# Kernel optimization log

Measured on AMD Instinct MI355X. Metric: run time of the kernel, lower is better.

Reference implementation:

```python
import jax, jax.numpy as jnp
import numpy as np


def _sliding_window_attention(q, k, v, window_size, padding_mask):
    # q,k,v: [B,H,S,D]; faithful to the torch code incl. clamped scatter_add
    # duplicates at boundaries and the (score==0 -> -inf) quirk.
    B, H, S, D = q.shape
    hw = window_size // 2
    kp = jnp.pad(k, ((0, 0), (0, 0), (hw, hw), (0, 0)))  # zero-pad seq dim
    # window gather positions into padded keys: [S, W+1]
    pos = jnp.arange(S)[:, None] + jnp.arange(window_size + 1)[None, :]
    kw = kp[:, :, pos, :]  # [B,H,S,W+1,D]
    scores = jnp.einsum('bhsd,bhswd->bhsw', q, kw) / jnp.sqrt(jnp.asarray(D, q.dtype))
    # scatter-add into full [B,H,S,S] with clamped column indices (duplicates sum)
    idx = jnp.clip(jnp.arange(S)[:, None] + jnp.arange(-hw, hw + 1)[None, :], 0, S - 1)  # [S,W+1]
    rows = jnp.arange(S)[:, None]
    full = jnp.zeros((B, H, S, S), q.dtype).at[:, :, rows, idx].add(scores)
    neg_inf = jnp.asarray(-jnp.inf, full.dtype)
    full = jnp.where(full == 0.0, neg_inf, full)
    if padding_mask is not None:
        pm = padding_mask[:, None, None, :]  # [B,1,1,S]
        full = jnp.where(pm == 0, neg_inf, full)
        full = jnp.where(jnp.swapaxes(pm, -1, -2) == 0, neg_inf, full)
    att = jax.nn.softmax(full, axis=-1)
    att = jnp.where(jnp.isnan(att), jnp.asarray(0.0, att.dtype), att)
    values = jnp.einsum('bhst,bhtd->bhsd', att, v)
    return values, att


def setup_inputs() -> dict:
    key = jax.random.key(0)
    ks = jax.random.split(key, 5)
    B, S, IN_DIM, E = 2, 2048, 512, 512
    x = jax.random.normal(ks[0], (B, S, IN_DIM), dtype=jnp.float32)
    padding_mask = jnp.ones((B, S), dtype=jnp.int32)
    qkv_w = jax.random.normal(ks[1], (3 * E, IN_DIM), dtype=jnp.float32) * 0.02
    qkv_b = jnp.zeros((3 * E,), dtype=jnp.float32)
    o_w = jax.random.normal(ks[2], (E, E), dtype=jnp.float32) * 0.02
    o_b = jnp.zeros((E,), dtype=jnp.float32)
    return {'x': x, 'padding_mask': padding_mask, 'qkv_w': qkv_w, 'qkv_b': qkv_b,
            'o_w': o_w, 'o_b': o_b, 'window_size': 256, 'num_heads': 8}


def reference(x, padding_mask, qkv_w, qkv_b, o_w, o_b, window_size, num_heads):
    B, S, _ = x.shape
    E3 = qkv_w.shape[0]
    E = E3 // 3
    head_dim = E // num_heads
    qkv = x @ qkv_w.T + qkv_b                         # [B,S,3E]
    qkv = qkv.reshape(B, S, num_heads, 3 * head_dim)
    qkv = jnp.transpose(qkv, (0, 2, 1, 3))            # [B,H,S,3*hd]
    q, k, v = jnp.split(qkv, 3, axis=-1)
    values, _ = _sliding_window_attention(q, k, v, window_size, padding_mask)
    values = jnp.transpose(values, (0, 2, 1, 3)).reshape(B, S, E)
    o = values @ o_w.T + o_b
    return o
```

## Files before the change

### kernel.cpp

```cpp
#include <hip/hip_runtime.h>
#include <hip/hip_bf16.h>
#include <math.h>


typedef __bf16 bf16x8 __attribute__((ext_vector_type(8)));
typedef float f32x4 __attribute__((ext_vector_type(4)));

__device__ __forceinline__ unsigned short f2bf(float f) {
  unsigned u = __float_as_uint(f);
  unsigned r = u + 0x7FFFu + ((u >> 16) & 1u);
  return (unsigned short)(r >> 16);
}

__device__ __forceinline__ void ldsdma16(void* lds, const void* g) {
  __builtin_amdgcn_global_load_lds(
      (const __attribute__((address_space(1))) unsigned int*)g,
      (__attribute__((address_space(3))) unsigned int*)lds, 16, 0, 0);
}

__global__ __launch_bounds__(256) void cvt3_kernel(
    const float* __restrict__ s0, unsigned short* __restrict__ d0, int n0,
    const float* __restrict__ s1, unsigned short* __restrict__ d1, int n1,
    const float* __restrict__ s2, unsigned short* __restrict__ d2, int n2) {
  int i4 = blockIdx.x * 256 + threadIdx.x;
  const int c0 = n0 >> 2, c1 = (n0 + n1) >> 2, c2 = (n0 + n1 + n2) >> 2;
  const float* s; unsigned short* d; int base4;
  if (i4 < c0)      { s = s0; d = d0; base4 = i4; }
  else if (i4 < c1) { s = s1; d = d1; base4 = i4 - c0; }
  else if (i4 < c2) { s = s2; d = d2; base4 = i4 - c1; }
  else return;
  float4 v = ((const float4*)s)[base4];
  ushort4 o;
  o.x = f2bf(v.x); o.y = f2bf(v.y); o.z = f2bf(v.z); o.w = f2bf(v.w);
  ((ushort4*)d)[base4] = o;
}

__global__ __launch_bounds__(256) void gemm_qkv(
    const __hip_bfloat16* __restrict__ A, const __hip_bfloat16* __restrict__ Bw,
    const float* __restrict__ bias,
    __hip_bfloat16* __restrict__ qp, __hip_bfloat16* __restrict__ kpb,
    unsigned short* __restrict__ vtb) {
  __shared__ __hip_bfloat16 As[128 * 32];
  __shared__ __hip_bfloat16 Bs[128 * 32];

  const int tid = threadIdx.x, wave = tid >> 6, lane = tid & 63;
  const int m0 = blockIdx.x * 128, n0 = blockIdx.y * 128;
  const int wm = (wave >> 1) * 64, wn = (wave & 1) * 64;
  const int cl = lane & 15, ko = (lane >> 4) * 8;
  const int srow = wave * 16 + (lane >> 2);
  const int scol = (lane & 3) * 8;

  f32x4 acc[4][4] = {};

  for (int k0 = 0; k0 < 512; k0 += 32) {
    __syncthreads();
    ldsdma16(&As[wave * 512],        A  + (size_t)(m0 + srow) * 512 + k0 + scol);
    ldsdma16(&As[2048 + wave * 512], A  + (size_t)(m0 + 64 + srow) * 512 + k0 + scol);
    ldsdma16(&Bs[wave * 512],        Bw + (size_t)(n0 + srow) * 512 + k0 + scol);
    ldsdma16(&Bs[2048 + wave * 512], Bw + (size_t)(n0 + 64 + srow) * 512 + k0 + scol);
    __syncthreads();

    bf16x8 af[4], bf[4];
#pragma unroll
    for (int i = 0; i < 4; i++)
      af[i] = *(const bf16x8*)(&As[(wm + cl + i * 16) * 32 + ko]);
#pragma unroll
    for (int i = 0; i < 4; i++)
      bf[i] = *(const bf16x8*)(&Bs[(wn + cl + i * 16) * 32 + ko]);
#pragma unroll
    for (int mi = 0; mi < 4; mi++)
#pragma unroll
      for (int ni = 0; ni < 4; ni++)
        acc[mi][ni] = __builtin_amdgcn_mfma_f32_16x16x32_bf16(
            af[mi], bf[ni], acc[mi][ni], 0, 0, 0);
  }

  const int crow = (lane >> 4) * 4;
#pragma unroll
  for (int mi = 0; mi < 4; mi++) {
    const int mb = m0 + wm + mi * 16 + crow;
    const int bq = mb >> 11, sl = mb & 2047;
#pragma unroll
    for (int ni = 0; ni < 4; ni++) {
      const int n = n0 + wn + ni * 16 + cl;
      const int h = n / 192;
      const int rem = n - h * 192;
      const int cat = rem >> 6;
      const int d = rem & 63;
      const float bv = bias[n];
      const size_t bh = (size_t)bq * 8 + h;
      if (cat == 2) {
        ushort4 o;
        o.x = f2bf(acc[mi][ni][0] + bv);
        o.y = f2bf(acc[mi][ni][1] + bv);
        o.z = f2bf(acc[mi][ni][2] + bv);
        o.w = f2bf(acc[mi][ni][3] + bv);
        *(ushort4*)(vtb + bh * 131072 + (sl >> 3) * 512 + d * 8 + (sl & 7)) = o;
      } else {
        __hip_bfloat16* dst = (cat == 0) ? qp : kpb;
        const float sc = (cat == 0) ? 0.18033688011112042f : 1.0f;
#pragma unroll
        for (int r = 0; r < 4; r++)
          dst[(bh * 2048 + sl + r) * 64 + d] =
              __float2bfloat16((acc[mi][ni][r] + bv) * sc);
      }
    }
  }
}

__global__ __launch_bounds__(256) void attn_mfma(
    const __hip_bfloat16* __restrict__ qp, const __hip_bfloat16* __restrict__ kp,
    const __hip_bfloat16* __restrict__ vt, const int* __restrict__ pm,
    __hip_bfloat16* __restrict__ vals) {
  __shared__ __hip_bfloat16 sKP[320 * 72];
  __shared__ float sCM[320];

  const int tid = threadIdx.x, wave = tid >> 6, lane = tid & 63;
  const int bid = blockIdx.x;
  const int s0 = (bid & 31) * 64;
  const int bh = bid >> 5;
  const int b = bh >> 3, h = bh & 7;
  const int t0 = s0 - 128;
  const int cl = lane & 15;
  const int g4 = (lane >> 4) * 4;
  const int ko = (lane >> 4) * 8;

  {
    const int e = (tid & 7) * 8;
#pragma unroll
    for (int i = 0; i < 10; i++) {
      int row = (tid >> 3) + i * 32;
      int t = t0 + row; t = min(max(t, 0), 2047);
      *(uint4*)(&sKP[row * 72 + e]) =
          *(const uint4*)(kp + ((size_t)bh * 2048 + t) * 64 + e);
    }
  }
  for (int c = tid; c < 320; c += 256) {
    int t = t0 + c;
    bool ok = (t >= 0 && t < 2048) && (pm[b * 2048 + t] != 0);
    sCM[c] = ok ? 0.0f : -3.0e38f;
  }
  __syncthreads();

  const __hip_bfloat16* qrow =
      qp + ((size_t)bh * 2048 + s0 + wave * 16 + cl) * 64 + ko;
  bf16x8 aq0 = *(const bf16x8*)(qrow);
  bf16x8 aq1 = *(const bf16x8*)(qrow + 32);

  f32x4 acc[17];
#pragma unroll
  for (int i = 0; i < 17; i++) {
    const int krow = (wave + i) * 16 + cl;
    bf16x8 b0 = *(const bf16x8*)(&sKP[krow * 72 + ko]);
    bf16x8 b1 = *(const bf16x8*)(&sKP[krow * 72 + ko + 32]);
    f32x4 z = {};
    z = __builtin_amdgcn_mfma_f32_16x16x32_bf16(aq0, b0, z, 0, 0, 0);
    acc[i] = __builtin_amdgcn_mfma_f32_16x16x32_bf16(aq1, b1, z, 0, 0, 0);
  }

  float mrow[4] = {-3.0e38f, -3.0e38f, -3.0e38f, -3.0e38f};
#pragma unroll
  for (int i = 0; i < 17; i++) {
    const float ca = sCM[(wave + i) * 16 + cl];
#pragma unroll
    for (int r = 0; r < 4; r++) {
      float sv = acc[i][r] + ca;
      if (i == 0) {
        if (cl < g4 + r) sv = -3.0e38f;
      } else if (i == 16) {
        if (cl > g4 + r) sv = -3.0e38f;
      }
      acc[i][r] = sv;
      mrow[r] = fmaxf(mrow[r], sv);
    }
  }
#pragma unroll
  for (int r = 0; r < 4; r++)
#pragma unroll
    for (int off = 1; off < 16; off <<= 1)
      mrow[r] = fmaxf(mrow[r], __shfl_xor(mrow[r], off));

  float lsum[4] = {0.f, 0.f, 0.f, 0.f};
#pragma unroll
  for (int i = 0; i < 17; i++)
#pragma unroll
    for (int r = 0; r < 4; r++) {
      float p = exp2f(acc[i][r] - mrow[r]);
      acc[i][r] = p;
      lsum[r] += p;
    }
#pragma unroll
  for (int r = 0; r < 4; r++)
#pragma unroll
    for (int off = 1; off < 16; off <<= 1)
      lsum[r] += __shfl_xor(lsum[r], off);

  __syncthreads();

  __hip_bfloat16* sp = sKP + wave * 5248;
#pragma unroll
  for (int i = 0; i < 17; i++) {
    const int c = (wave + i) * 16 + cl;
#pragma unroll
    for (int r = 0; r < 4; r++)
      sp[(g4 + r) * 328 + c] = __float2bfloat16(acc[i][r]);
  }
  {
    const int zt = (wave & 1) ? (wave - 1) : (wave + 17);
    const int zc = zt * 16 + cl;
#pragma unroll
    for (int r = 0; r < 4; r++)
      sp[(g4 + r) * 328 + zc] = __float2bfloat16(0.f);
  }

  f32x4 oacc[4] = {};
  const int k0 = wave >> 1;
  const __hip_bfloat16* vbase = vt + (size_t)bh * 131072;
#pragma unroll
  for (int ks = 0; ks < 9; ks++) {
    const int kk = (k0 + ks) * 32 + ko;
    bf16x8 pa = *(const bf16x8*)(&sp[cl * 328 + kk]);
    int tv = t0 + kk; tv = min(max(tv, 0), 2040);
    const __hip_bfloat16* vrow = vbase + (tv >> 3) * 512;
#pragma unroll
    for (int ni = 0; ni < 4; ni++) {
      const int d = ni * 16 + cl;
      bf16x8 vb = *(const bf16x8*)(vrow + d * 8);
      oacc[ni] = __builtin_amdgcn_mfma_f32_16x16x32_bf16(pa, vb, oacc[ni], 0, 0, 0);
    }
  }

#pragma unroll
  for (int r = 0; r < 4; r++) {
    float linv = 1.0f / fmaxf(lsum[r], 1e-20f);
    const int qr = wave * 16 + g4 + r;
    if (sCM[qr + 128] != 0.0f) linv = 0.0f;
    const size_t obase = ((size_t)(b * 2048 + s0 + qr)) * 512 + h * 64 + cl;
#pragma unroll
    for (int ni = 0; ni < 4; ni++)
      vals[obase + ni * 16] = __float2bfloat16(oacc[ni][r] * linv);
  }
}

__global__ __launch_bounds__(256) void gemm_out(
    const __hip_bfloat16* __restrict__ A, const __hip_bfloat16* __restrict__ Bw,
    const float* __restrict__ bias, float* __restrict__ C) {
  __shared__ __hip_bfloat16 As[64 * 32];
  __shared__ __hip_bfloat16 Bs[128 * 32];

  const int tid = threadIdx.x, wave = tid >> 6, lane = tid & 63;
  const int m0 = blockIdx.x * 64, n0 = blockIdx.y * 128;
  const int wm = (wave >> 1) * 32, wn = (wave & 1) * 64;
  const int cl = lane & 15, ko = (lane >> 4) * 8;
  const int srow = wave * 16 + (lane >> 2);
  const int scol = (lane & 3) * 8;

  f32x4 acc[2][4] = {};

  for (int k0 = 0; k0 < 512; k0 += 32) {
    __syncthreads();
    ldsdma16(&As[wave * 512],        A  + (size_t)(m0 + srow) * 512 + k0 + scol);
    ldsdma16(&Bs[wave * 512],        Bw + (size_t)(n0 + srow) * 512 + k0 + scol);
    ldsdma16(&Bs[2048 + wave * 512], Bw + (size_t)(n0 + 64 + srow) * 512 + k0 + scol);
    __syncthreads();

    bf16x8 af[2], bf[4];
#pragma unroll
    for (int i = 0; i < 2; i++)
      af[i] = *(const bf16x8*)(&As[(wm + cl + i * 16) * 32 + ko]);
#pragma unroll
    for (int i = 0; i < 4; i++)
      bf[i] = *(const bf16x8*)(&Bs[(wn + cl + i * 16) * 32 + ko]);
#pragma unroll
    for (int mi = 0; mi < 2; mi++)
#pragma unroll
      for (int ni = 0; ni < 4; ni++)
        acc[mi][ni] = __builtin_amdgcn_mfma_f32_16x16x32_bf16(
            af[mi], bf[ni], acc[mi][ni], 0, 0, 0);
  }

  const int crow = (lane >> 4) * 4;
#pragma unroll
  for (int mi = 0; mi < 2; mi++) {
#pragma unroll
    for (int ni = 0; ni < 4; ni++) {
      const int n = n0 + wn + ni * 16 + cl;
      const float bv = bias[n];
      const int mb = m0 + wm + mi * 16 + crow;
#pragma unroll
      for (int r = 0; r < 4; r++)
        C[(size_t)(mb + r) * 512 + n] = acc[mi][ni][r] + bv;
    }
  }
}

extern "C" void kernel_launch(void* const* d_in, const int* in_sizes, int n_in,
                              void* d_out, int out_size, void* d_ws, size_t ws_size,
                              hipStream_t stream) {
  const float* x     = (const float*)d_in[0];
  const int*   pm    = (const int*)d_in[1];
  const float* qkv_w = (const float*)d_in[2];
  const float* qkv_b = (const float*)d_in[3];
  const float* o_w   = (const float*)d_in[4];
  const float* o_b   = (const float*)d_in[5];
  float* out = (float*)d_out;

  __hip_bfloat16* wsb   = (__hip_bfloat16*)d_ws;
  __hip_bfloat16* xb    = wsb;
  __hip_bfloat16* wqkvb = wsb + 2097152;
  __hip_bfloat16* wob   = wsb + 2883584;
  __hip_bfloat16* qp    = wsb + 3145728;
  __hip_bfloat16* kp    = wsb + 5242880;
  __hip_bfloat16* vt    = wsb + 7340032;
  __hip_bfloat16* vals  = wsb + 9437184;

  dim3 blk(256);
  cvt3_kernel<<<dim3(3072), blk, 0, stream>>>(
      x, (unsigned short*)xb, 2097152,
      qkv_w, (unsigned short*)wqkvb, 786432,
      o_w, (unsigned short*)wob, 262144);
  gemm_qkv<<<dim3(32, 12), blk, 0, stream>>>(
      xb, wqkvb, qkv_b, qp, kp, (unsigned short*)vt);
  attn_mfma<<<dim3(512), blk, 0, stream>>>(qp, kp, vt, pm, vals);
  gemm_out<<<dim3(64, 4), blk, 0, stream>>>(vals, wob, o_b, out);
}
```

Baseline: 114.5 us.

## Fuse all four stages into one cooperative persistent kernel with grid syncs

Replaces the four separate launches (convert, QKV GEMM, attention, output GEMM) with a single cooperative kernel of 512 blocks. The stages are separated by grid-wide barriers, and the original launches remain as a fallback if the cooperative launch fails. The aim is to remove per-launch overhead and the gaps between kernels. In exchange, the GEMM stages use only 384 or 256 of the 512 blocks, and each grid sync adds its own barrier latency.

```diff
diff --git a/kernel.cpp b/kernel.cpp
--- a/kernel.cpp
+++ b/kernel.cpp
@@ -1,6 +1,9 @@
 #include <hip/hip_runtime.h>
 #include <hip/hip_bf16.h>
+#include <hip/hip_cooperative_groups.h>
 #include <math.h>
+
+namespace cg = cooperative_groups;
 
 
 typedef __bf16 bf16x8 __attribute__((ext_vector_type(8)));
@@ -16,6 +19,286 @@
   __builtin_amdgcn_global_load_lds(
       (const __attribute__((address_space(1))) unsigned int*)g,
       (__attribute__((address_space(3))) unsigned int*)lds, 16, 0, 0);
+}
+
+__global__ __launch_bounds__(256, 2) void fused_all(
+    const float* __restrict__ x, const int* __restrict__ pm,
+    const float* __restrict__ qkv_w, const float* __restrict__ qkv_b,
+    const float* __restrict__ o_w, const float* __restrict__ o_b,
+    float* __restrict__ out,
+    __hip_bfloat16* __restrict__ xb, __hip_bfloat16* __restrict__ wqkvb,
+    __hip_bfloat16* __restrict__ wob,
+    __hip_bfloat16* __restrict__ qp, __hip_bfloat16* __restrict__ kp,
+    __hip_bfloat16* __restrict__ vt, __hip_bfloat16* __restrict__ vals) {
+  __shared__ __align__(16) unsigned char smem[320 * 72 * 2 + 320 * 4];
+
+  const int tid = threadIdx.x, bid = blockIdx.x;
+  const int wave = tid >> 6, lane = tid & 63;
+
+  {
+    const int gtid = bid * 256 + tid;
+#pragma unroll
+    for (int it = 0; it < 6; it++) {
+      const int i4 = gtid + it * 131072;
+      const float* s; unsigned short* d; int b4;
+      if (i4 < 524288)      { s = x;     d = (unsigned short*)xb;    b4 = i4; }
+      else if (i4 < 720896) { s = qkv_w; d = (unsigned short*)wqkvb; b4 = i4 - 524288; }
+      else                  { s = o_w;   d = (unsigned short*)wob;   b4 = i4 - 720896; }
+      float4 v = ((const float4*)s)[b4];
+      ushort4 o;
+      o.x = f2bf(v.x); o.y = f2bf(v.y); o.z = f2bf(v.z); o.w = f2bf(v.w);
+      ((ushort4*)d)[b4] = o;
+    }
+  }
+  cg::this_grid().sync();
+
+  if (bid < 384) {
+    __hip_bfloat16* As = (__hip_bfloat16*)smem;
+    __hip_bfloat16* Bs = As + 4096;
+    const int m0 = (bid & 31) * 128, n0 = (bid >> 5) * 128;
+    const int wm = (wave >> 1) * 64, wn = (wave & 1) * 64;
+    const int cl = lane & 15, ko = (lane >> 4) * 8;
+    const int srow = wave * 16 + (lane >> 2);
+    const int scol = (lane & 3) * 8;
+
+    f32x4 acc[4][4] = {};
+
+    for (int k0 = 0; k0 < 512; k0 += 32) {
+      __syncthreads();
+      ldsdma16(&As[wave * 512],        xb    + (size_t)(m0 + srow) * 512 + k0 + scol);
+      ldsdma16(&As[2048 + wave * 512], xb    + (size_t)(m0 + 64 + srow) * 512 + k0 + scol);
+      ldsdma16(&Bs[wave * 512],        wqkvb + (size_t)(n0 + srow) * 512 + k0 + scol);
+      ldsdma16(&Bs[2048 + wave * 512], wqkvb + (size_t)(n0 + 64 + srow) * 512 + k0 + scol);
+      __syncthreads();
+
+      bf16x8 af[4], bf[4];
+#pragma unroll
+      for (int i = 0; i < 4; i++)
+        af[i] = *(const bf16x8*)(&As[(wm + cl + i * 16) * 32 + ko]);
+#pragma unroll
+      for (int i = 0; i < 4; i++)
+        bf[i] = *(const bf16x8*)(&Bs[(wn + cl + i * 16) * 32 + ko]);
+#pragma unroll
+      for (int mi = 0; mi < 4; mi++)
+#pragma unroll
+        for (int ni = 0; ni < 4; ni++)
+          acc[mi][ni] = __builtin_amdgcn_mfma_f32_16x16x32_bf16(
+              af[mi], bf[ni], acc[mi][ni], 0, 0, 0);
+    }
+
+    unsigned short* vtb = (unsigned short*)vt;
+    const int crow = (lane >> 4) * 4;
+#pragma unroll
+    for (int mi = 0; mi < 4; mi++) {
+      const int mb = m0 + wm + mi * 16 + crow;
+      const int bq = mb >> 11, sl = mb & 2047;
+#pragma unroll
+      for (int ni = 0; ni < 4; ni++) {
+        const int n = n0 + wn + ni * 16 + cl;
+        const int h = n / 192;
+        const int rem = n - h * 192;
+        const int cat = rem >> 6;
+        const int d = rem & 63;
+        const float bv = qkv_b[n];
+        const size_t bh = (size_t)bq * 8 + h;
+        if (cat == 2) {
+          ushort4 o;
+          o.x = f2bf(acc[mi][ni][0] + bv);
+          o.y = f2bf(acc[mi][ni][1] + bv);
+          o.z = f2bf(acc[mi][ni][2] + bv);
+          o.w = f2bf(acc[mi][ni][3] + bv);
+          *(ushort4*)(vtb + bh * 131072 + (sl >> 3) * 512 + d * 8 + (sl & 7)) = o;
+        } else {
+          __hip_bfloat16* dst = (cat == 0) ? qp : kp;
+          const float sc = (cat == 0) ? 0.18033688011112042f : 1.0f;
+#pragma unroll
+          for (int r = 0; r < 4; r++)
+            dst[(bh * 2048 + sl + r) * 64 + d] =
+                __float2bfloat16((acc[mi][ni][r] + bv) * sc);
+        }
+      }
+    }
+  }
+  cg::this_grid().sync();
+
+  {
+    __hip_bfloat16* sKP = (__hip_bfloat16*)smem;
+    float* sCM = (float*)(smem + 46080);
+
+    const int s0 = (bid & 31) * 64;
+    const int bh = bid >> 5;
+    const int b = bh >> 3;
+    const int t0 = s0 - 128;
+    const int cl = lane & 15;
+    const int g4 = (lane >> 4) * 4;
+    const int ko = (lane >> 4) * 8;
+
+    {
+      const int e = (tid & 7) * 8;
+#pragma unroll
+      for (int i = 0; i < 10; i++) {
+        int row = (tid >> 3) + i * 32;
+        int t = t0 + row; t = min(max(t, 0), 2047);
+        *(uint4*)(&sKP[row * 72 + e]) =
+            *(const uint4*)(kp + ((size_t)bh * 2048 + t) * 64 + e);
+      }
+    }
+    for (int c = tid; c < 320; c += 256) {
+      int t = t0 + c;
+      bool ok = (t >= 0 && t < 2048) && (pm[b * 2048 + t] != 0);
+      sCM[c] = ok ? 0.0f : -3.0e38f;
+    }
+    __syncthreads();
+
+    const __hip_bfloat16* qrow =
+        qp + ((size_t)bh * 2048 + s0 + wave * 16 + cl) * 64 + ko;
+    bf16x8 aq0 = *(const bf16x8*)(qrow);
+    bf16x8 aq1 = *(const bf16x8*)(qrow + 32);
+
+    f32x4 acc[17];
+#pragma unroll
+    for (int i = 0; i < 17; i++) {
+      const int krow = (wave + i) * 16 + cl;
+      bf16x8 b0 = *(const bf16x8*)(&sKP[krow * 72 + ko]);
+      bf16x8 b1 = *(const bf16x8*)(&sKP[krow * 72 + ko + 32]);
+      f32x4 z = {};
+      z = __builtin_amdgcn_mfma_f32_16x16x32_bf16(aq0, b0, z, 0, 0, 0);
+      acc[i] = __builtin_amdgcn_mfma_f32_16x16x32_bf16(aq1, b1, z, 0, 0, 0);
+    }
+
+    float mrow[4] = {-3.0e38f, -3.0e38f, -3.0e38f, -3.0e38f};
+#pragma unroll
+    for (int i = 0; i < 17; i++) {
+      const float ca = sCM[(wave + i) * 16 + cl];
+#pragma unroll
+      for (int r = 0; r < 4; r++) {
+        float sv = acc[i][r] + ca;
+        if (i == 0) {
+          if (cl < g4 + r) sv = -3.0e38f;
+        } else if (i == 16) {
+          if (cl > g4 + r) sv = -3.0e38f;
+        }
+        acc[i][r] = sv;
+        mrow[r] = fmaxf(mrow[r], sv);
+      }
+    }
+#pragma unroll
+    for (int r = 0; r < 4; r++)
+#pragma unroll
+      for (int off = 1; off < 16; off <<= 1)
+        mrow[r] = fmaxf(mrow[r], __shfl_xor(mrow[r], off));
+
+    float lsum[4] = {0.f, 0.f, 0.f, 0.f};
+#pragma unroll
+    for (int i = 0; i < 17; i++)
+#pragma unroll
+      for (int r = 0; r < 4; r++) {
+        float p = exp2f(acc[i][r] - mrow[r]);
+        acc[i][r] = p;
+        lsum[r] += p;
+      }
+#pragma unroll
+    for (int r = 0; r < 4; r++)
+#pragma unroll
+      for (int off = 1; off < 16; off <<= 1)
+        lsum[r] += __shfl_xor(lsum[r], off);
+
+    __syncthreads();
+
+    __hip_bfloat16* sp = sKP + wave * 5248;
+#pragma unroll
+    for (int i = 0; i < 17; i++) {
+      const int c = (wave + i) * 16 + cl;
+#pragma unroll
+      for (int r = 0; r < 4; r++)
+        sp[(g4 + r) * 328 + c] = __float2bfloat16(acc[i][r]);
+    }
+    {
+      const int zt = (wave & 1) ? (wave - 1) : (wave + 17);
+      const int zc = zt * 16 + cl;
+#pragma unroll
+      for (int r = 0; r < 4; r++)
+        sp[(g4 + r) * 328 + zc] = __float2bfloat16(0.f);
+    }
+
+    f32x4 oacc[4] = {};
+    const int k0 = wave >> 1;
+    const __hip_bfloat16* vbase = vt + (size_t)bh * 131072;
+#pragma unroll
+    for (int ks = 0; ks < 9; ks++) {
+      const int kk = (k0 + ks) * 32 + ko;
+      bf16x8 pa = *(const bf16x8*)(&sp[cl * 328 + kk]);
+      int tv = t0 + kk; tv = min(max(tv, 0), 2040);
+      const __hip_bfloat16* vrow = vbase + (tv >> 3) * 512;
+#pragma unroll
+      for (int ni = 0; ni < 4; ni++) {
+        const int d = ni * 16 + cl;
+        bf16x8 vb = *(const bf16x8*)(vrow + d * 8);
+        oacc[ni] = __builtin_amdgcn_mfma_f32_16x16x32_bf16(pa, vb, oacc[ni], 0, 0, 0);
+      }
+    }
+
+    const int h = bh & 7;
+#pragma unroll
+    for (int r = 0; r < 4; r++) {
+      float linv = 1.0f / fmaxf(lsum[r], 1e-20f);
+      const int qr = wave * 16 + g4 + r;
+      if (sCM[qr + 128] != 0.0f) linv = 0.0f;
+      const size_t obase = ((size_t)(b * 2048 + s0 + qr)) * 512 + h * 64 + cl;
+#pragma unroll
+      for (int ni = 0; ni < 4; ni++)
+        vals[obase + ni * 16] = __float2bfloat16(oacc[ni][r] * linv);
+    }
+  }
+  cg::this_grid().sync();
+
+  if (bid < 256) {
+    __hip_bfloat16* As = (__hip_bfloat16*)smem;
+    __hip_bfloat16* Bs = As + 2048;
+    const int m0 = (bid & 63) * 64, n0 = (bid >> 6) * 128;
+    const int wm = (wave >> 1) * 32, wn = (wave & 1) * 64;
+    const int cl = lane & 15, ko = (lane >> 4) * 8;
+    const int srow = wave * 16 + (lane >> 2);
+    const int scol = (lane & 3) * 8;
+
+    f32x4 acc[2][4] = {};
+
+    for (int k0 = 0; k0 < 512; k0 += 32) {
+      __syncthreads();
+      ldsdma16(&As[wave * 512],        vals + (size_t)(m0 + srow) * 512 + k0 + scol);
+      ldsdma16(&Bs[wave * 512],        wob  + (size_t)(n0 + srow) * 512 + k0 + scol);
+      ldsdma16(&Bs[2048 + wave * 512], wob  + (size_t)(n0 + 64 + srow) * 512 + k0 + scol);
+      __syncthreads();
+
+      bf16x8 af[2], bf[4];
+#pragma unroll
+      for (int i = 0; i < 2; i++)
+        af[i] = *(const bf16x8*)(&As[(wm + cl + i * 16) * 32 + ko]);
+#pragma unroll
+      for (int i = 0; i < 4; i++)
+        bf[i] = *(const bf16x8*)(&Bs[(wn + cl + i * 16) * 32 + ko]);
+#pragma unroll
+      for (int mi = 0; mi < 2; mi++)
+#pragma unroll
+        for (int ni = 0; ni < 4; ni++)
+          acc[mi][ni] = __builtin_amdgcn_mfma_f32_16x16x32_bf16(
+              af[mi], bf[ni], acc[mi][ni], 0, 0, 0);
+    }
+
+    const int crow = (lane >> 4) * 4;
+#pragma unroll
+    for (int mi = 0; mi < 2; mi++) {
+#pragma unroll
+      for (int ni = 0; ni < 4; ni++) {
+        const int n = n0 + wn + ni * 16 + cl;
+        const float bv = o_b[n];
+        const int mb = m0 + wm + mi * 16 + crow;
+#pragma unroll
+        for (int r = 0; r < 4; r++)
+          out[(size_t)(mb + r) * 512 + n] = acc[mi][ni][r] + bv;
+      }
+    }
+  }
 }
 
 __global__ __launch_bounds__(256) void cvt3_kernel(
@@ -314,13 +597,22 @@
   __hip_bfloat16* vt    = wsb + 7340032;
   __hip_bfloat16* vals  = wsb + 9437184;
 
-  dim3 blk(256);
-  cvt3_kernel<<<dim3(3072), blk, 0, stream>>>(
-      x, (unsigned short*)xb, 2097152,
-      qkv_w, (unsigned short*)wqkvb, 786432,
-      o_w, (unsigned short*)wob, 262144);
-  gemm_qkv<<<dim3(32, 12), blk, 0, stream>>>(
-      xb, wqkvb, qkv_b, qp, kp, (unsigned short*)vt);
-  attn_mfma<<<dim3(512), blk, 0, stream>>>(qp, kp, vt, pm, vals);
-  gemm_out<<<dim3(64, 4), blk, 0, stream>>>(vals, wob, o_b, out);
-}
+  void* args[] = {(void*)&x,     (void*)&pm,   (void*)&qkv_w, (void*)&qkv_b,
+                  (void*)&o_w,   (void*)&o_b,  (void*)&out,
+                  (void*)&xb,    (void*)&wqkvb,(void*)&wob,
+                  (void*)&qp,    (void*)&kp,   (void*)&vt,    (void*)&vals};
+  hipError_t err = hipLaunchCooperativeKernel(
+      reinterpret_cast<void*>(&fused_all), dim3(512), dim3(256), args, 0, stream);
+
+  if (err != hipSuccess) {
+    dim3 blk(256);
+    cvt3_kernel<<<dim3(3072), blk, 0, stream>>>(
+        x, (unsigned short*)xb, 2097152,
+        qkv_w, (unsigned short*)wqkvb, 786432,
+        o_w, (unsigned short*)wob, 262144);
+    gemm_qkv<<<dim3(32, 12), blk, 0, stream>>>(
+        xb, wqkvb, qkv_b, qp, kp, (unsigned short*)vt);
+    attn_mfma<<<dim3(512), blk, 0, stream>>>(qp, kp, vt, pm, vals);
+    gemm_out<<<dim3(64, 4), blk, 0, stream>>>(vals, wob, o_b, out);
+  }
+}
```

Result: slower. 305.6 us (+167.0%).
